# Optimization experiments

Hardware: AMD Instinct MI355X
Metric: run time of the kernel (lower is better)

## Reference

```python
import jax, jax.numpy as jnp
import numpy as np

B, N, L, H, K = 65536, 32, 8, 256, 8
RMIN, RMAX = -10.0, 10.0
MIN_BIN, MIN_SLOPE = 1e-4, 1e-4
P = 3 * K + 1  # params per feature per spline


def setup_inputs() -> dict:
    key = jax.random.key(0)
    ks = jax.random.split(key, 20)
    def rn(k, shape, s=0.05):
        return (jax.random.normal(k, shape, dtype=jnp.float32) * s)
    inp = {
        'x': jax.random.normal(ks[0], (B, N), dtype=jnp.float32),
        'sc_scale': 1.0 + rn(ks[1], (L, N)),
        'sc_shift': rn(ks[2], (L, N)),
        'W_in': rn(ks[3], (L, N, H)), 'b_in': rn(ks[4], (L, H)),
        'W1a': rn(ks[5], (L, H, H)), 'b1a': rn(ks[6], (L, H)),
        'W1b': rn(ks[7], (L, H, H)), 'b1b': rn(ks[8], (L, H)),
        'W2a': rn(ks[9], (L, H, H)), 'b2a': rn(ks[10], (L, H)),
        'W2b': rn(ks[11], (L, H, H)), 'b2b': rn(ks[12], (L, H)),
        'W_out': rn(ks[13], (L, H, N * P)), 'b_out': rn(ks[14], (L, N * P)),
        'perms': jnp.asarray(np.stack([np.random.RandomState(i).permutation(N) for i in range(L)]).astype(np.int32)),
    }
    return inp


def _conditioner(mx, Wi, bi, W1a, b1a, W1b, b1b, W2a, b2a, W2b, b2b, Wo, bo):
    # mx: [B, N] masked input -> [B, N, P] spline params
    h = mx @ Wi + bi
    r = jax.nn.relu(jax.nn.relu(h @ W1a + b1a) @ W1b + b1b)
    h = h + r
    r = jax.nn.relu(jax.nn.relu(h @ W2a + b2a) @ W2b + b2b)
    h = h + r
    h = jax.nn.relu(h)
    out = h @ Wo + bo
    return out.reshape(mx.shape[0], N, P)


def _rqs_forward(x, params):
    # x: [B, N]; params: [B, N, 3K+1]. distrax RationalQuadraticSpline forward.
    uw, uh, ud = params[..., :K], params[..., K:2 * K], params[..., 2 * K:]
    total = RMAX - RMIN
    w = jax.nn.softmax(uw, axis=-1) * (total - K * MIN_BIN) + MIN_BIN
    hgt = jax.nn.softmax(uh, axis=-1) * (total - K * MIN_BIN) + MIN_BIN
    zpad = jnp.zeros_like(w[..., :1])
    xp = RMIN + jnp.concatenate([zpad, jnp.cumsum(w, -1)], -1)   # [B,N,K+1]
    yp = RMIN + jnp.concatenate([zpad, jnp.cumsum(hgt, -1)], -1)
    offset = float(np.log(np.expm1(1.0 - MIN_SLOPE)))
    d = jax.nn.softplus(ud + offset) + MIN_SLOPE                  # [B,N,K+1]
    inside = (x > RMIN) & (x < RMAX)
    xc = jnp.clip(x, RMIN, RMAX)
    # per-element bin search (knot positions vary per element)
    idx = jnp.clip(jnp.sum((xc[..., None] >= xp).astype(jnp.int32), -1) - 1, 0, K - 1)
    g = lambda a, i: jnp.take_along_axis(a, i[..., None], -1)[..., 0]
    xk, xk1 = g(xp, idx), g(xp, idx + 1)
    yk, yk1 = g(yp, idx), g(yp, idx + 1)
    dk, dk1 = g(d, idx), g(d, idx + 1)
    bw = xk1 - xk
    bh = yk1 - yk
    s = bh / bw
    z = jnp.clip((xc - xk) / bw, 0.0, 1.0)
    zz = z * (1.0 - z)
    denom = s + (dk1 + dk - 2.0 * s) * zz
    y = yk + bh * (s * z * z + dk * zz) / denom
    ld = 2.0 * jnp.log(s) + jnp.log(dk1 * z * z + 2.0 * s * zz + dk * (1.0 - z) ** 2) - 2.0 * jnp.log(denom)
    return jnp.where(inside, y, x), jnp.where(inside, ld, 0.0)


def reference(x, sc_scale, sc_shift, W_in, b_in, W1a, b1a, W1b, b1b,
              W2a, b2a, W2b, b2b, W_out, b_out, perms):
    mask0 = (jnp.arange(N) % 2).astype(bool)  # True = identity (masked)
    logdet = jnp.zeros(x.shape[0], dtype=x.dtype)
    for i in range(L):
        # Permute
        x = x[:, perms[i]]
        # Scalar affine on all features (mask_all = all-False coupling)
        x = x * sc_scale[i] + sc_shift[i]
        logdet = logdet + jnp.sum(jnp.log(jnp.abs(sc_scale[i])))
        # RQ-spline masked coupling
        mask = mask0 if i % 2 == 0 else ~mask0
        mx = jnp.where(mask, x, 0.0)
        params = _conditioner(mx, W_in[i], b_in[i], W1a[i], b1a[i], W1b[i], b1b[i],
                              W2a[i], b2a[i], W2b[i], b2b[i], W_out[i], b_out[i])
        y, ld = _rqs_forward(x, params)
        x = jnp.where(mask, x, y)
        logdet = logdet + jnp.sum(jnp.where(mask, 0.0, ld), axis=-1)
    # standard-normal base log prob
    logp = -0.5 * jnp.sum(x * x, axis=-1) - 0.5 * N * float(np.log(2.0 * np.pi))
    return logp + logdet
```

## Files before the change

kernel.cpp:

```cpp
#include <hip/hip_runtime.h>
#include <hip/hip_bf16.h>

typedef __attribute__((ext_vector_type(8))) short bf16x8;
typedef __attribute__((ext_vector_type(16))) float f32x16;
typedef __attribute__((ext_vector_type(2))) float f32x2;

#define DEVFN __device__ __forceinline__

constexpr int NFEAT = 32, NLAYER = 8, HID = 256;
constexpr int HS  = 264;
constexpr int MXS = 40;
constexpr int XS  = 33;
constexpr int WIN_E  = 2 * 256 * 16;
constexpr int WH_E   = 16 * 256 * 16;
constexpr int WOUT_E = 16 * 512 * 16;
constexpr int LAYER_E = WIN_E + 4 * WH_E + WOUT_E;
constexpr size_t WT_BYTES = (size_t)LAYER_E * NLAYER * 2;
constexpr size_t CPERM_OFF = WT_BYTES + (size_t)NLAYER * 512 * 4 + 4;
constexpr size_t WS_NEEDED = CPERM_OFF + (size_t)NLAYER * 32 * 4;

constexpr float MIN_BIN = 1e-4f, MIN_SLOPE = 1e-4f;
constexpr float SOFTPLUS_OFF = 0.5411666f;
constexpr float WSCALE = 20.0f - 8.0f * MIN_BIN;

DEVFN unsigned short bf16r(float f) {
    unsigned u = __float_as_uint(f);
    u += 0x7fffu + ((u >> 16) & 1u);
    return (unsigned short)(u >> 16);
}
#if defined(__gfx950__) && __has_builtin(__builtin_amdgcn_cvt_pk_bf16_f32)
DEVFN unsigned pack2(float a, float b) {
    auto r = __builtin_amdgcn_cvt_pk_bf16_f32(a, b);
    return __builtin_bit_cast(unsigned, r);
}
#else
DEVFN unsigned pack2(float a, float b) {
    return (unsigned)bf16r(a) | ((unsigned)bf16r(b) << 16);
}
#endif
DEVFN float bflo(unsigned v) { return __uint_as_float(v << 16); }
DEVFN float bfhi(unsigned v) { return __uint_as_float(v & 0xffff0000u); }
DEVFN float frcp(float x) { return __builtin_amdgcn_rcpf(x); }
DEVFN f32x2 vmax0(f32x2 v) {
#if __has_builtin(__builtin_elementwise_max)
    return __builtin_elementwise_max(v, (f32x2){0.f, 0.f});
#else
    return (f32x2){fmaxf(v.x, 0.f), fmaxf(v.y, 0.f)};
#endif
}

__global__ __launch_bounds__(256) void prep_kernel(
    const float* __restrict__ Win, const float* __restrict__ W1a, const float* __restrict__ W1b,
    const float* __restrict__ W2a, const float* __restrict__ W2b, const float* __restrict__ Wout,
    const float* __restrict__ bout, const float* __restrict__ scS,
    const int* __restrict__ perms,
    short* __restrict__ wt, float* __restrict__ bo_t, float* __restrict__ sld,
    int* __restrict__ cperm)
{
    __shared__ float lb[16 * 800];
    const int b = blockIdx.x, t = threadIdx.x;
    if (b < 16) {
        int l = b >> 1, ks = b & 1;
        const float* src = Win + l * 32 * 256 + ks * 16 * 256;
#pragma unroll
        for (int i = 0; i < 16; i++) { int idx = t + i * 256; lb[idx] = src[idx]; }
        __syncthreads();
        short* dst = wt + (size_t)l * LAYER_E + ks * 4096;
#pragma unroll
        for (int i = 0; i < 16; i++) {
            int o = t + i * 256; int n = o >> 4, kk = o & 15;
            dst[o] = (short)bf16r(lb[kk * 256 + n]);
        }
    } else if (b < 528) {
        int id = b - 16; int l = id >> 6, mat = (id >> 4) & 3, ks = id & 15;
        const float* mats[4] = {W1a, W1b, W2a, W2b};
        const float* src = mats[mat] + l * 65536 + ks * 16 * 256;
#pragma unroll
        for (int i = 0; i < 16; i++) { int idx = t + i * 256; lb[idx] = src[idx]; }
        __syncthreads();
        short* dst = wt + (size_t)l * LAYER_E + WIN_E + mat * WH_E + ks * 4096;
#pragma unroll
        for (int i = 0; i < 16; i++) {
            int o = t + i * 256; int n = o >> 4, kk = o & 15;
            dst[o] = (short)bf16r(lb[kk * 256 + n]);
        }
    } else if (b < 656) {
        int id = b - 528; int l = id >> 4, ks = id & 15; int par = l & 1;
        const float* src = Wout + (size_t)l * 256 * 800 + ks * 16 * 800;
        for (int k = 0; k < 16; k++)
            for (int c = t; c < 800; c += 256) lb[k * 800 + c] = src[k * 800 + c];
        __syncthreads();
        short* dst = wt + (size_t)l * LAYER_E + WIN_E + 4 * WH_E + ks * 8192;
#pragma unroll
        for (int i = 0; i < 32; i++) {
            int o = t + i * 256; int c = o >> 4, kk = o & 15;
            int u = c >> 5, p = c & 31;
            float v = (p < 25) ? lb[kk * 800 + (2 * u + par) * 25 + p] : 0.0f;
            dst[o] = (short)bf16r(v);
        }
    } else {
        if (t == 0) {
            for (int j = 0; j < 32; j++) cperm[j] = perms[j];
            for (int l = 1; l < NLAYER; l++)
                for (int j = 0; j < 32; j++)
                    cperm[l * 32 + j] = cperm[(l - 1) * 32 + perms[l * 32 + j]];
        }
#pragma unroll
        for (int i = 0; i < 16; i++) {
            int idx = t + i * 256;
            int l = idx >> 9, c = idx & 511, u = c >> 5, p = c & 31;
            bo_t[idx] = (p < 25) ? bout[l * 800 + (2 * u + (l & 1)) * 25 + p] : 0.0f;
        }
        lb[t] = logf(fabsf(scS[t]));
        __syncthreads();
        for (int s = 128; s > 0; s >>= 1) { if (t < s) lb[t] += lb[t + s]; __syncthreads(); }
        if (t == 0) *sld = lb[0];
    }
}

template<int D, int NSUB>
DEVFN void prefA(const short* __restrict__ wt, int ntot, int nbase, bf16x8 (&a)[D][NSUB])
{
    const int lane = threadIdx.x & 63;
    const bf16x8* __restrict__ w8 = (const bf16x8*)wt;
    const int wb = (nbase + (lane & 31)) * 2 + (lane >> 5);
    const int krow = ntot * 2;
#pragma unroll
    for (int p = 0; p < D; p++)
#pragma unroll
        for (int s = 0; s < NSUB; s++)
            a[p][s] = w8[(size_t)p * krow + wb + s * 64];
}

template<int KSTEPS, int NSUB, int D>
DEVFN void gemm_run(const short* __restrict__ wt, int ntot, int nbase,
                    const unsigned short* __restrict__ B, int bs,
                    bf16x8 (&a)[D][NSUB], f32x16 (&acc)[NSUB][2])
{
    const int lane = threadIdx.x & 63;
    const int l31 = lane & 31, l5 = lane >> 5;
    const bf16x8* __restrict__ w8 = (const bf16x8*)wt;
    const int wb = (nbase + l31) * 2 + l5;
    const int krow = ntot * 2;
    const unsigned short* bp = B + l31 * bs + l5 * 8;
#pragma unroll
    for (int k = 0; k < KSTEPS; k++) {
        bf16x8 b0 = *(const bf16x8*)(bp + k * 16);
        bf16x8 b1 = *(const bf16x8*)(bp + 32 * bs + k * 16);
#pragma unroll
        for (int s = 0; s < NSUB; s++) {
            acc[s][0] = __builtin_amdgcn_mfma_f32_32x32x16_bf16(a[k % D][s], b0, acc[s][0], 0, 0, 0);
            acc[s][1] = __builtin_amdgcn_mfma_f32_32x32x16_bf16(a[k % D][s], b1, acc[s][1], 0, 0, 0);
        }
        if (k + D < KSTEPS) {
#pragma unroll
            for (int s = 0; s < NSUB; s++) a[k % D][s] = w8[(size_t)(k + D) * krow + wb + s * 64];
        }
    }
}

DEVFN void binit(f32x16& a, const float* __restrict__ bias)
{
    const int q = (threadIdx.x >> 5) & 1;
    const float* bp = bias + 4 * q;
#pragma unroll
    for (int g = 0; g < 4; g++) {
        float4 b = *(const float4*)(bp + 8 * g);
        a[4*g+0] = b.x; a[4*g+1] = b.y; a[4*g+2] = b.z; a[4*g+3] = b.w;
    }
}

template<int MODE>
DEVFN void store_h(const f32x16& v, unsigned short* buf, int m0, int n0)
{
    const int lane = threadIdx.x & 63;
    const int m = m0 + (lane & 31);
    const int q = lane >> 5;
    unsigned short* rowp = buf + m * HS + n0 + 4 * q;
#pragma unroll
    for (int g = 0; g < 4; g++) {
        f32x2 r0 = {v[4*g+0], v[4*g+1]};
        f32x2 r1 = {v[4*g+2], v[4*g+3]};
        if (MODE >= 1) { r0 = vmax0(r0); r1 = vmax0(r1); }
        unsigned short* dst = rowp + 8 * g;
        if (MODE >= 2) {
            uint2 old = *(const uint2*)dst;
            r0 += (f32x2){bflo(old.x), bfhi(old.x)};
            r1 += (f32x2){bflo(old.y), bfhi(old.y)};
            if (MODE == 3) { r0 = vmax0(r0); r1 = vmax0(r1); }
        }
        uint2 pk;
        pk.x = pack2(r0.x, r0.y);
        pk.y = pack2(r1.x, r1.y);
        *(uint2*)dst = pk;
    }
}

__global__ __launch_bounds__(256, 2) void flow_kernel(
    const float* __restrict__ x_in, const float* __restrict__ scS, const float* __restrict__ scB,
    const float* __restrict__ bin, const float* __restrict__ b1a, const float* __restrict__ b1b,
    const float* __restrict__ b2a, const float* __restrict__ b2b,
    const int* __restrict__ cperm,
    const short* __restrict__ wt, const float* __restrict__ bo_t, const float* __restrict__ sld,
    float* __restrict__ out)
{
    __shared__ __align__(16) unsigned short hS[64 * HS];
    __shared__ __align__(16) unsigned short uS[64 * HS];
    __shared__ float xS[64 * XS];
    __shared__ float redS[256];

    const int tid = threadIdx.x;
    const int wave = tid >> 6;
    const int lane = tid & 63;
    const int q = lane >> 5;
    const size_t rowbase = (size_t)blockIdx.x * 64;
    unsigned short* tS  = uS;
    unsigned short* mxS = uS;

#pragma unroll
    for (int i = 0; i < 8; i++) {
        int g = tid + i * 256;
        xS[(g >> 5) * XS + (g & 31)] = x_in[rowbase * NFEAT + g];
    }
    float ld_acc = 0.0f;
    __syncthreads();

    const int nbase = wave * 64;
    bf16x8 rG1[2][2];
    bf16x8 rB[8][2];
    bf16x8 rW[2][4];

#pragma unroll 1
    for (int l = 0; l < NLAYER; l++) {
        const int par = l & 1;
        const short* wb = wt + (size_t)l * LAYER_E;

        {
            int j = tid & 31; int r0 = (tid >> 5) * 8;
            int cj = cperm[l * 32 + j];
            float sc = scS[l * 32 + j], sh = scB[l * 32 + j];
            int keep = ((j & 1) != par);
#pragma unroll
            for (int r = 0; r < 8; r++) {
                float v = fmaf(xS[(r0 + r) * XS + cj], sc, sh);
                xS[(r0 + r) * XS + cj] = v;
                mxS[(r0 + r) * MXS + j] = keep ? bf16r(v) : (unsigned short)0;
            }
        }
        prefA<2, 2>(wb, 256, nbase, rG1);
        __syncthreads();
        {
            f32x16 acc[2][2];
            binit(acc[0][0], bin + l * 256 + nbase);      binit(acc[0][1], bin + l * 256 + nbase);
            binit(acc[1][0], bin + l * 256 + nbase + 32); binit(acc[1][1], bin + l * 256 + nbase + 32);
            gemm_run<2, 2, 2>(wb, 256, nbase, mxS, MXS, rG1, acc);
            prefA<8, 2>(wb + WIN_E, 256, nbase, rB);
#pragma unroll
            for (int s = 0; s < 2; s++) {
                store_h<0>(acc[s][0], hS, 0,  nbase + s * 32);
                store_h<0>(acc[s][1], hS, 32, nbase + s * 32);
            }
            __syncthreads();
        }
        {
            f32x16 acc[2][2];
            binit(acc[0][0], b1a + l * 256 + nbase);      binit(acc[0][1], b1a + l * 256 + nbase);
            binit(acc[1][0], b1a + l * 256 + nbase + 32); binit(acc[1][1], b1a + l * 256 + nbase + 32);
            gemm_run<16, 2, 8>(wb + WIN_E, 256, nbase, hS, HS, rB, acc);
            prefA<8, 2>(wb + WIN_E + WH_E, 256, nbase, rB);
#pragma unroll
            for (int s = 0; s < 2; s++) {
                store_h<1>(acc[s][0], tS, 0,  nbase + s * 32);
                store_h<1>(acc[s][1], tS, 32, nbase + s * 32);
            }
            __syncthreads();
        }
        {
            f32x16 acc[2][2];
            binit(acc[0][0], b1b + l * 256 + nbase);      binit(acc[0][1], b1b + l * 256 + nbase);
            binit(acc[1][0], b1b + l * 256 + nbase + 32); binit(acc[1][1], b1b + l * 256 + nbase + 32);
            gemm_run<16, 2, 8>(wb + WIN_E + WH_E, 256, nbase, tS, HS, rB, acc);
            prefA<8, 2>(wb + WIN_E + 2 * WH_E, 256, nbase, rB);
#pragma unroll
            for (int s = 0; s < 2; s++) {
                store_h<2>(acc[s][0], hS, 0,  nbase + s * 32);
                store_h<2>(acc[s][1], hS, 32, nbase + s * 32);
            }
            __syncthreads();
        }
        {
            f32x16 acc[2][2];
            binit(acc[0][0], b2a + l * 256 + nbase);      binit(acc[0][1], b2a + l * 256 + nbase);
            binit(acc[1][0], b2a + l * 256 + nbase + 32); binit(acc[1][1], b2a + l * 256 + nbase + 32);
            gemm_run<16, 2, 8>(wb + WIN_E + 2 * WH_E, 256, nbase, hS, HS, rB, acc);
            prefA<8, 2>(wb + WIN_E + 3 * WH_E, 256, nbase, rB);
#pragma unroll
            for (int s = 0; s < 2; s++) {
                store_h<1>(acc[s][0], tS, 0,  nbase + s * 32);
                store_h<1>(acc[s][1], tS, 32, nbase + s * 32);
            }
            __syncthreads();
        }
        {
            f32x16 acc[2][2];
            binit(acc[0][0], b2b + l * 256 + nbase);      binit(acc[0][1], b2b + l * 256 + nbase);
            binit(acc[1][0], b2b + l * 256 + nbase + 32); binit(acc[1][1], b2b + l * 256 + nbase + 32);
            gemm_run<16, 2, 8>(wb + WIN_E + 3 * WH_E, 256, nbase, tS, HS, rB, acc);
            prefA<2, 4>(wb + WIN_E + 4 * WH_E, 512, wave * 128, rW);
#pragma unroll
            for (int s = 0; s < 2; s++) {
                store_h<3>(acc[s][0], hS, 0,  nbase + s * 32);
                store_h<3>(acc[s][1], hS, 32, nbase + s * 32);
            }
            __syncthreads();
        }
        {
            const short* wo = wb + WIN_E + 4 * WH_E;
            f32x16 acc[4][2];
            const float* bb = bo_t + l * 512 + wave * 128;
#pragma unroll
            for (int s = 0; s < 4; s++) { binit(acc[s][0], bb + s * 32); binit(acc[s][1], bb + s * 32); }
            gemm_run<16, 4, 2>(wo, 512, wave * 128, hS, HS, rW, acc);

#pragma unroll
            for (int s = 0; s < 4; s++) {
                float exch[16];
#pragma unroll
                for (int i = 0; i < 16; i++) {
                    float snd = q ? acc[s][0][i] : acc[s][1][i];
                    exch[i] = __shfl_xor(snd, 32, 64);
                }
                float A0[16], A1[16];
#pragma unroll
                for (int i = 0; i < 16; i++) {
                    float kept = q ? acc[s][1][i] : acc[s][0][i];
                    A0[i] = q ? exch[i] : kept;
                    A1[i] = q ? kept : exch[i];
                }
                float P[25];
#pragma unroll
                for (int p = 0; p < 25; p++) {
                    int rg = (p & 3) + 4 * (p >> 3);
                    P[p] = ((p >> 2) & 1) ? A1[rg] : A0[rg];
                }
                int n = 2 * (4 * wave + s) + par;
                int cn = cperm[l * 32 + n];
                float xv = xS[lane * XS + cn];
                float ew[8], eh[8], sw = 0.f, sh2 = 0.f;
#pragma unroll
                for (int i = 0; i < 8; i++) { ew[i] = __expf(P[i]); sw += ew[i]; }
#pragma unroll
                for (int i = 0; i < 8; i++) { eh[i] = __expf(P[8 + i]); sh2 += eh[i]; }
                float fw = WSCALE * frcp(sw), fh = WSCALE * frcp(sh2);
                float w[8], hh[8];
#pragma unroll
                for (int i = 0; i < 8; i++) { w[i] = fmaf(ew[i], fw, MIN_BIN); hh[i] = fmaf(eh[i], fh, MIN_BIN); }

                bool inside = (xv > -10.0f) && (xv < 10.0f);
                float xc = fminf(fmaxf(xv, -10.0f), 10.0f);
                float cx = -10.0f + w[0], cy = -10.0f + hh[0];
                float xk = -10.0f, yk = -10.0f, bw = w[0], bh = hh[0];
                float udk = P[16], udk1 = P[17];
#pragma unroll
                for (int i = 1; i < 8; i++) {
                    bool take = (xc >= cx);
                    if (take) { xk = cx; yk = cy; bw = w[i]; bh = hh[i]; udk = P[16 + i]; udk1 = P[17 + i]; }
                    cx += w[i]; cy += hh[i];
                }
                float dk  = __logf(1.f + __expf(udk  + SOFTPLUS_OFF)) + MIN_SLOPE;
                float dk1 = __logf(1.f + __expf(udk1 + SOFTPLUS_OFF)) + MIN_SLOPE;
                float ibw = frcp(bw);
                float s_ = bh * ibw;
                float z = fminf(fmaxf((xc - xk) * ibw, 0.0f), 1.0f);
                float omz = 1.0f - z;
                float zz = z * omz;
                float denom = fmaf(dk1 + dk - 2.0f * s_, zz, s_);
                float idenom = frcp(denom);
                float y = fmaf(bh * fmaf(s_ * z, z, dk * zz), idenom, yk);
                float num = fmaf(dk1 * z, z, fmaf(2.0f * s_, zz, dk * omz * omz));
                float t1 = s_ * idenom;
                float ldv = __logf(t1 * t1 * num);
                xS[lane * XS + cn] = inside ? y : xv;
                ld_acc += inside ? ldv : 0.0f;
            }
            __syncthreads();
        }
    }
    {
        int m = tid & 63, jg = tid >> 6;
        float s2 = 0.f;
#pragma unroll
        for (int j = 0; j < 8; j++) { float v = xS[m * XS + jg * 8 + j]; s2 += v * v; }
        redS[tid] = ld_acc - 0.5f * s2;
        __syncthreads();
        if (tid < 64) {
            float tot = redS[tid] + redS[tid + 64] + redS[tid + 128] + redS[tid + 192]
                      + *sld - 29.406033062549525f;
            out[rowbase + tid] = tot;
        }
    }
}

extern "C" void kernel_launch(void* const* d_in, const int* in_sizes, int n_in,
                              void* d_out, int out_size, void* d_ws, size_t ws_size,
                              hipStream_t stream) {
    if (ws_size < WS_NEEDED) return;
    const float* x    = (const float*)d_in[0];
    const float* scS  = (const float*)d_in[1];
    const float* scB  = (const float*)d_in[2];
    const float* Win  = (const float*)d_in[3];
    const float* bin  = (const float*)d_in[4];
    const float* W1a  = (const float*)d_in[5];
    const float* b1a  = (const float*)d_in[6];
    const float* W1b  = (const float*)d_in[7];
    const float* b1b  = (const float*)d_in[8];
    const float* W2a  = (const float*)d_in[9];
    const float* b2a  = (const float*)d_in[10];
    const float* W2b  = (const float*)d_in[11];
    const float* b2b  = (const float*)d_in[12];
    const float* Wout = (const float*)d_in[13];
    const float* bout = (const float*)d_in[14];
    const int* perms  = (const int*)d_in[15];

    short* wt   = (short*)d_ws;
    float* bo_t = (float*)((char*)d_ws + WT_BYTES);
    float* sld  = bo_t + NLAYER * 512;
    int* cperm  = (int*)((char*)d_ws + CPERM_OFF);

    prep_kernel<<<657, 256, 0, stream>>>(Win, W1a, W1b, W2a, W2b, Wout, bout, scS, perms,
                                         wt, bo_t, sld, cperm);
    flow_kernel<<<65536 / 64, 256, 0, stream>>>(x, scS, scB, bin, b1a, b1b, b2a, b2b,
                                                cperm, wt, bo_t, sld, (float*)d_out);
}
```

Baseline: 598.9 us.

## Split per-block work across 8 waves instead of 4

Doubles the block to 512 threads (8 waves), so each wave computes half as many output columns in every GEMM stage and the output projection runs as two sequential 32-column passes. The goal is more waves for latency hiding and fewer registers per wave for weight prefetch buffers and accumulators. The cost is more barrier participants, smaller per-wave MFMA tiles with less B-operand reuse, and launch bounds asking for 4 blocks per CU, which LDS capacity (about 76 KB per block) may not allow.

```diff
diff --git a/kernel.cpp b/kernel.cpp
--- a/kernel.cpp
+++ b/kernel.cpp
@@ -196,7 +196,7 @@
     }
 }
 
-__global__ __launch_bounds__(256, 2) void flow_kernel(
+__global__ __launch_bounds__(512, 4) void flow_kernel(
     const float* __restrict__ x_in, const float* __restrict__ scS, const float* __restrict__ scB,
     const float* __restrict__ bin, const float* __restrict__ b1a, const float* __restrict__ b1b,
     const float* __restrict__ b2a, const float* __restrict__ b2b,
@@ -207,7 +207,7 @@
     __shared__ __align__(16) unsigned short hS[64 * HS];
     __shared__ __align__(16) unsigned short uS[64 * HS];
     __shared__ float xS[64 * XS];
-    __shared__ float redS[256];
+    __shared__ float redS[512];
 
     const int tid = threadIdx.x;
     const int wave = tid >> 6;
@@ -218,17 +218,17 @@
     unsigned short* mxS = uS;
 
 #pragma unroll
-    for (int i = 0; i < 8; i++) {
-        int g = tid + i * 256;
+    for (int i = 0; i < 4; i++) {
+        int g = tid + i * 512;
         xS[(g >> 5) * XS + (g & 31)] = x_in[rowbase * NFEAT + g];
     }
     float ld_acc = 0.0f;
     __syncthreads();
 
-    const int nbase = wave * 64;
-    bf16x8 rG1[2][2];
-    bf16x8 rB[8][2];
-    bf16x8 rW[2][4];
+    const int nbase = wave * 32;
+    bf16x8 rG1[2][1];
+    bf16x8 rB[8][1];
+    bf16x8 rW[2][1];
 
 #pragma unroll 1
     for (int l = 0; l < NLAYER; l++) {
@@ -236,104 +236,90 @@
         const short* wb = wt + (size_t)l * LAYER_E;
 
         {
-            int j = tid & 31; int r0 = (tid >> 5) * 8;
+            int j = tid & 31; int r0 = (tid >> 5) * 4;
             int cj = cperm[l * 32 + j];
             float sc = scS[l * 32 + j], sh = scB[l * 32 + j];
             int keep = ((j & 1) != par);
 #pragma unroll
-            for (int r = 0; r < 8; r++) {
+            for (int r = 0; r < 4; r++) {
                 float v = fmaf(xS[(r0 + r) * XS + cj], sc, sh);
                 xS[(r0 + r) * XS + cj] = v;
                 mxS[(r0 + r) * MXS + j] = keep ? bf16r(v) : (unsigned short)0;
             }
         }
-        prefA<2, 2>(wb, 256, nbase, rG1);
-        __syncthreads();
-        {
-            f32x16 acc[2][2];
-            binit(acc[0][0], bin + l * 256 + nbase);      binit(acc[0][1], bin + l * 256 + nbase);
-            binit(acc[1][0], bin + l * 256 + nbase + 32); binit(acc[1][1], bin + l * 256 + nbase + 32);
-            gemm_run<2, 2, 2>(wb, 256, nbase, mxS, MXS, rG1, acc);
-            prefA<8, 2>(wb + WIN_E, 256, nbase, rB);
+        prefA<2, 1>(wb, 256, nbase, rG1);
+        __syncthreads();
+        {
+            f32x16 acc[1][2];
+            binit(acc[0][0], bin + l * 256 + nbase);
+            binit(acc[0][1], bin + l * 256 + nbase);
+            gemm_run<2, 1, 2>(wb, 256, nbase, mxS, MXS, rG1, acc);
+            prefA<8, 1>(wb + WIN_E, 256, nbase, rB);
+            store_h<0>(acc[0][0], hS, 0,  nbase);
+            store_h<0>(acc[0][1], hS, 32, nbase);
+            __syncthreads();
+        }
+        {
+            f32x16 acc[1][2];
+            binit(acc[0][0], b1a + l * 256 + nbase);
+            binit(acc[0][1], b1a + l * 256 + nbase);
+            gemm_run<16, 1, 8>(wb + WIN_E, 256, nbase, hS, HS, rB, acc);
+            prefA<8, 1>(wb + WIN_E + WH_E, 256, nbase, rB);
+            store_h<1>(acc[0][0], tS, 0,  nbase);
+            store_h<1>(acc[0][1], tS, 32, nbase);
+            __syncthreads();
+        }
+        {
+            f32x16 acc[1][2];
+            binit(acc[0][0], b1b + l * 256 + nbase);
+            binit(acc[0][1], b1b + l * 256 + nbase);
+            gemm_run<16, 1, 8>(wb + WIN_E + WH_E, 256, nbase, tS, HS, rB, acc);
+            prefA<8, 1>(wb + WIN_E + 2 * WH_E, 256, nbase, rB);
+            store_h<2>(acc[0][0], hS, 0,  nbase);
+            store_h<2>(acc[0][1], hS, 32, nbase);
+            __syncthreads();
+        }
+        {
+            f32x16 acc[1][2];
+            binit(acc[0][0], b2a + l * 256 + nbase);
+            binit(acc[0][1], b2a + l * 256 + nbase);
+            gemm_run<16, 1, 8>(wb + WIN_E + 2 * WH_E, 256, nbase, hS, HS, rB, acc);
+            prefA<8, 1>(wb + WIN_E + 3 * WH_E, 256, nbase, rB);
+            store_h<1>(acc[0][0], tS, 0,  nbase);
+            store_h<1>(acc[0][1], tS, 32, nbase);
+            __syncthreads();
+        }
+        {
+            f32x16 acc[1][2];
+            binit(acc[0][0], b2b + l * 256 + nbase);
+            binit(acc[0][1], b2b + l * 256 + nbase);
+            gemm_run<16, 1, 8>(wb + WIN_E + 3 * WH_E, 256, nbase, tS, HS, rB, acc);
+            prefA<2, 1>(wb + WIN_E + 4 * WH_E, 512, wave * 64, rW);
+            store_h<3>(acc[0][0], hS, 0,  nbase);
+            store_h<3>(acc[0][1], hS, 32, nbase);
+            __syncthreads();
+        }
+        {
+            const short* wo = wb + WIN_E + 4 * WH_E;
 #pragma unroll
             for (int s = 0; s < 2; s++) {
-                store_h<0>(acc[s][0], hS, 0,  nbase + s * 32);
-                store_h<0>(acc[s][1], hS, 32, nbase + s * 32);
-            }
-            __syncthreads();
-        }
-        {
-            f32x16 acc[2][2];
-            binit(acc[0][0], b1a + l * 256 + nbase);      binit(acc[0][1], b1a + l * 256 + nbase);
-            binit(acc[1][0], b1a + l * 256 + nbase + 32); binit(acc[1][1], b1a + l * 256 + nbase + 32);
-            gemm_run<16, 2, 8>(wb + WIN_E, 256, nbase, hS, HS, rB, acc);
-            prefA<8, 2>(wb + WIN_E + WH_E, 256, nbase, rB);
-#pragma unroll
-            for (int s = 0; s < 2; s++) {
-                store_h<1>(acc[s][0], tS, 0,  nbase + s * 32);
-                store_h<1>(acc[s][1], tS, 32, nbase + s * 32);
-            }
-            __syncthreads();
-        }
-        {
-            f32x16 acc[2][2];
-            binit(acc[0][0], b1b + l * 256 + nbase);      binit(acc[0][1], b1b + l * 256 + nbase);
-            binit(acc[1][0], b1b + l * 256 + nbase + 32); binit(acc[1][1], b1b + l * 256 + nbase + 32);
-            gemm_run<16, 2, 8>(wb + WIN_E + WH_E, 256, nbase, tS, HS, rB, acc);
-            prefA<8, 2>(wb + WIN_E + 2 * WH_E, 256, nbase, rB);
-#pragma unroll
-            for (int s = 0; s < 2; s++) {
-                store_h<2>(acc[s][0], hS, 0,  nbase + s * 32);
-                store_h<2>(acc[s][1], hS, 32, nbase + s * 32);
-            }
-            __syncthreads();
-        }
-        {
-            f32x16 acc[2][2];
-            binit(acc[0][0], b2a + l * 256 + nbase);      binit(acc[0][1], b2a + l * 256 + nbase);
-            binit(acc[1][0], b2a + l * 256 + nbase + 32); binit(acc[1][1], b2a + l * 256 + nbase + 32);
-            gemm_run<16, 2, 8>(wb + WIN_E + 2 * WH_E, 256, nbase, hS, HS, rB, acc);
-            prefA<8, 2>(wb + WIN_E + 3 * WH_E, 256, nbase, rB);
-#pragma unroll
-            for (int s = 0; s < 2; s++) {
-                store_h<1>(acc[s][0], tS, 0,  nbase + s * 32);
-                store_h<1>(acc[s][1], tS, 32, nbase + s * 32);
-            }
-            __syncthreads();
-        }
-        {
-            f32x16 acc[2][2];
-            binit(acc[0][0], b2b + l * 256 + nbase);      binit(acc[0][1], b2b + l * 256 + nbase);
-            binit(acc[1][0], b2b + l * 256 + nbase + 32); binit(acc[1][1], b2b + l * 256 + nbase + 32);
-            gemm_run<16, 2, 8>(wb + WIN_E + 3 * WH_E, 256, nbase, tS, HS, rB, acc);
-            prefA<2, 4>(wb + WIN_E + 4 * WH_E, 512, wave * 128, rW);
-#pragma unroll
-            for (int s = 0; s < 2; s++) {
-                store_h<3>(acc[s][0], hS, 0,  nbase + s * 32);
-                store_h<3>(acc[s][1], hS, 32, nbase + s * 32);
-            }
-            __syncthreads();
-        }
-        {
-            const short* wo = wb + WIN_E + 4 * WH_E;
-            f32x16 acc[4][2];
-            const float* bb = bo_t + l * 512 + wave * 128;
-#pragma unroll
-            for (int s = 0; s < 4; s++) { binit(acc[s][0], bb + s * 32); binit(acc[s][1], bb + s * 32); }
-            gemm_run<16, 4, 2>(wo, 512, wave * 128, hS, HS, rW, acc);
-
-#pragma unroll
-            for (int s = 0; s < 4; s++) {
+                f32x16 acc[1][2];
+                const float* bb = bo_t + l * 512 + wave * 64 + s * 32;
+                binit(acc[0][0], bb);
+                binit(acc[0][1], bb);
+                gemm_run<16, 1, 2>(wo, 512, wave * 64 + s * 32, hS, HS, rW, acc);
+                if (s == 0) prefA<2, 1>(wo, 512, wave * 64 + 32, rW);
+
                 float exch[16];
 #pragma unroll
                 for (int i = 0; i < 16; i++) {
-                    float snd = q ? acc[s][0][i] : acc[s][1][i];
+                    float snd = q ? acc[0][0][i] : acc[0][1][i];
                     exch[i] = __shfl_xor(snd, 32, 64);
                 }
                 float A0[16], A1[16];
 #pragma unroll
                 for (int i = 0; i < 16; i++) {
-                    float kept = q ? acc[s][1][i] : acc[s][0][i];
+                    float kept = q ? acc[0][1][i] : acc[0][0][i];
                     A0[i] = q ? exch[i] : kept;
                     A1[i] = q ? kept : exch[i];
                 }
@@ -343,7 +329,7 @@
                     int rg = (p & 3) + 4 * (p >> 3);
                     P[p] = ((p >> 2) & 1) ? A1[rg] : A0[rg];
                 }
-                int n = 2 * (4 * wave + s) + par;
+                int n = 2 * (2 * wave + s) + par;
                 int cn = cperm[l * 32 + n];
                 float xv = xS[lane * XS + cn];
                 float ew[8], eh[8], sw = 0.f, sh2 = 0.f;
@@ -390,12 +376,13 @@
         int m = tid & 63, jg = tid >> 6;
         float s2 = 0.f;
 #pragma unroll
-        for (int j = 0; j < 8; j++) { float v = xS[m * XS + jg * 8 + j]; s2 += v * v; }
+        for (int j = 0; j < 4; j++) { float v = xS[m * XS + jg * 4 + j]; s2 += v * v; }
         redS[tid] = ld_acc - 0.5f * s2;
         __syncthreads();
         if (tid < 64) {
-            float tot = redS[tid] + redS[tid + 64] + redS[tid + 128] + redS[tid + 192]
-                      + *sld - 29.406033062549525f;
+            float tot = *sld - 29.406033062549525f;
+#pragma unroll
+            for (int k = 0; k < 8; k++) tot += redS[tid + 64 * k];
             out[rowbase + tid] = tot;
         }
     }
@@ -429,6 +416,6 @@
 
     prep_kernel<<<657, 256, 0, stream>>>(Win, W1a, W1b, W2a, W2b, Wout, bout, scS, perms,
                                          wt, bo_t, sld, cperm);
-    flow_kernel<<<65536 / 64, 256, 0, stream>>>(x, scS, scB, bin, b1a, b1b, b2a, b2b,
+    flow_kernel<<<65536 / 64, 512, 0, stream>>>(x, scS, scB, bin, b1a, b1b, b2a, b2b,
                                                 cperm, wt, bo_t, sld, (float*)d_out);
 }
```

Result: slower. 959.4 us (+60.2%).
